# Kernel optimization log

Measured on AMD Instinct MI355X. Metric: run time of the kernel, lower is better.

The kernel has to match this reference:

```python
import jax, jax.numpy as jnp
import numpy as np


def setup_inputs() -> dict:
    key = jax.random.key(0)
    k1, k2 = jax.random.split(key)
    B, C, H, W_, P = 32, 256, 64, 64, 8
    x = jax.random.normal(k1, (B, C, H, W_), dtype=jnp.float32)
    # 1x1 conv weight [P, C] and bias [P], init like torch Conv2d default
    bound = 1.0 / np.sqrt(C)
    W = jax.random.uniform(k2, (P, C), dtype=jnp.float32, minval=-bound, maxval=bound)
    b = jnp.zeros((P,), dtype=jnp.float32)
    return {"x": x, "W": W, "b": b}


def reference(x, W, b):
    B, C, H, Wd = x.shape
    P = W.shape[0]
    # 1x1 conv: scores[b,p,h,w] = sum_c W[p,c] * x[b,c,h,w] + b[p]
    scores = jnp.einsum('pc,bchw->bphw', W, x) + b[None, :, None, None]
    # spatial softmax over HW
    part_maps = jax.nn.softmax(scores.reshape(B, P, H * Wd), axis=2).reshape(B, P, H, Wd)
    # fused per-part weighted average pool: mean over HW of x * map
    pooled = jnp.einsum('bchw,bphw->bpc', x, part_maps) / (H * Wd)  # [B,P,C]
    return pooled.reshape(B, P * C)
```

## Files before the change

kernel.cpp:

```cpp
#include <hip/hip_runtime.h>

#define HW 4096
#define NC 256
#define NP 8
#define NB 32
#define CHW 32
#define CPB 4
#define SPAN 128
#define NSPAN 32
#define NBLK (NB * NSPAN)

#define FMA4(acc, v, s)                  \
  acc.x = fmaf((v).x, (s), acc.x);       \
  acc.y = fmaf((v).y, (s), acc.y);       \
  acc.z = fmaf((v).z, (s), acc.z);       \
  acc.w = fmaf((v).w, (s), acc.w)

__global__ __launch_bounds__(256) void k_fused(
    const float* __restrict__ x, const float* __restrict__ Wm,
    const float* __restrict__ bias, float* __restrict__ partial,
    float* __restrict__ psum) {
  __shared__ __align__(16) float xs[NC][CHW];
  __shared__ __align__(16) float wt[NC][NP];
  __shared__ __align__(16) float sp[4][NP][CHW];
  __shared__ __align__(16) float els[NP][CHW];

  const int bid = blockIdx.x;
  const int b = bid >> 5;
  const int span = bid & 31;
  const int t = threadIdx.x, lane = t & 63, w = t >> 6;
  const float* xb = x + (size_t)b * NC * HW + span * SPAN;

#pragma unroll
  for (int p = 0; p < NP; ++p) wt[t][p] = Wm[p * NC + t];

  const int cr = lane >> 3;
  const int q = lane & 7;
  const int c0 = w << 6;
  const int ep = t >> 5, eh = t & 31;
  const int tk = t & 7;
  const float* xwp = xb + (size_t)(c0 + cr) * HW + q * 4;
  const float bia = bias[ep];

  float pacc[NP];
#pragma unroll
  for (int p = 0; p < NP; ++p) pacc[p] = 0.f;
  float esum_tot = 0.f;

  __syncthreads();

#pragma unroll 1
  for (int k = 0; k < CPB; ++k) {
    if (k) __syncthreads();

    float4 xv[8];
#pragma unroll
    for (int i = 0; i < 8; ++i)
      xv[i] = *(const float4*)(xwp + k * CHW + (size_t)(i * 8) * HW);

    float4 s4[NP];
#pragma unroll
    for (int p = 0; p < NP; ++p) s4[p] = make_float4(0.f, 0.f, 0.f, 0.f);
#pragma unroll
    for (int i = 0; i < 8; ++i) {
      const int c = c0 + i * 8 + cr;
      *(float4*)&xs[c][(q ^ cr) * 4] = xv[i];
      const float4 wA = *(const float4*)&wt[c][0];
      const float4 wB = *(const float4*)&wt[c][4];
      FMA4(s4[0], xv[i], wA.x);
      FMA4(s4[1], xv[i], wA.y);
      FMA4(s4[2], xv[i], wA.z);
      FMA4(s4[3], xv[i], wA.w);
      FMA4(s4[4], xv[i], wB.x);
      FMA4(s4[5], xv[i], wB.y);
      FMA4(s4[6], xv[i], wB.z);
      FMA4(s4[7], xv[i], wB.w);
    }

#pragma unroll
    for (int p = 0; p < NP; ++p) {
      float4 v = s4[p];
      v.x += __shfl_xor(v.x, 8);  v.y += __shfl_xor(v.y, 8);
      v.z += __shfl_xor(v.z, 8);  v.w += __shfl_xor(v.w, 8);
      v.x += __shfl_xor(v.x, 16); v.y += __shfl_xor(v.y, 16);
      v.z += __shfl_xor(v.z, 16); v.w += __shfl_xor(v.w, 16);
      v.x += __shfl_xor(v.x, 32); v.y += __shfl_xor(v.y, 32);
      v.z += __shfl_xor(v.z, 32); v.w += __shfl_xor(v.w, 32);
      if (cr == 0) *(float4*)&sp[w][p][q * 4] = v;
    }
    __syncthreads();

    {
      float a = bia;
#pragma unroll
      for (int ww = 0; ww < 4; ++ww) a += sp[ww][ep][eh];
      float e0 = expf(a);
      els[ep][eh] = e0;
      esum_tot += e0;
    }
    __syncthreads();

#pragma unroll
    for (int j = 0; j < 8; ++j) {
      const float4 xvb = *(const float4*)&xs[t][(j ^ tk) * 4];
#pragma unroll
      for (int p = 0; p < NP; ++p) {
        const float4 e4 = *(const float4*)&els[p][j * 4];
        pacc[p] = fmaf(xvb.x, e4.x, pacc[p]);
        pacc[p] = fmaf(xvb.y, e4.y, pacc[p]);
        pacc[p] = fmaf(xvb.z, e4.z, pacc[p]);
        pacc[p] = fmaf(xvb.w, e4.w, pacc[p]);
      }
    }
  }

#pragma unroll
  for (int p = 0; p < NP; ++p)
    partial[((size_t)bid * NP + p) * NC + t] = pacc[p];

#pragma unroll
  for (int off = 16; off; off >>= 1) esum_tot += __shfl_xor(esum_tot, off);
  if (eh == 0) psum[bid * NP + ep] = esum_tot;
}

__global__ __launch_bounds__(256) void k_reduce(
    const float* __restrict__ partial, const float* __restrict__ psum,
    float* __restrict__ out) {
  int bp = blockIdx.x;
  int b = bp >> 3, p = bp & 7;
  int t = threadIdx.x, lane = t & 63, w2 = t >> 6;

  __shared__ float gv;
  if (w2 == 0) {
    float v = (lane < NSPAN) ? psum[(size_t)(b * NSPAN + lane) * NP + p] : 0.f;
#pragma unroll
    for (int off = 16; off; off >>= 1) v += __shfl_xor(v, off);
    if (lane == 0) gv = 1.0f / (v * (float)HW);
  }
  __syncthreads();
  float ginv = gv;

  float acc = 0.f;
#pragma unroll
  for (int i = 0; i < NSPAN; ++i)
    acc += partial[(((size_t)b * NSPAN + i) * NP + p) * NC + t];
  out[((size_t)b * NP + p) * NC + t] = acc * ginv;
}

extern "C" void kernel_launch(void* const* d_in, const int* in_sizes, int n_in,
                              void* d_out, int out_size, void* d_ws, size_t ws_size,
                              hipStream_t stream) {
  const float* x = (const float*)d_in[0];
  const float* Wm = (const float*)d_in[1];
  const float* bias = (const float*)d_in[2];
  float* out = (float*)d_out;

  float* ws = (float*)d_ws;
  float* partial = ws;
  float* psum = ws + (size_t)NBLK * NP * NC;

  k_fused<<<NBLK, 256, 0, stream>>>(x, Wm, bias, partial, psum);
  k_reduce<<<NB * NP, 256, 0, stream>>>(partial, psum, out);
}
```

Baseline: 56.45 us.

## Pipeline x loads via async global_load_lds with 4-stage LDS ring, 512-thread blocks

Replaces register-staged x loads with direct global-to-LDS async loads, keeping three chunks in flight across a four-buffer ring with manual vmcnt waits and raw barriers. Blocks become 512 threads, each covering 512 spatial positions in 16 chunks, so the grid drops from 1024 to 256 blocks and the partial buffer and reduce work shrink. The intent is to hide HBM latency behind compute. The cost is more LDS per block, fewer blocks for occupancy, and fragile hand-written waitcnt logic.

```diff
diff --git a/kernel.cpp b/kernel.cpp
--- a/kernel.cpp
+++ b/kernel.cpp
@@ -1,14 +1,14 @@
 #include <hip/hip_runtime.h>
+#include <stdint.h>
 
 #define HW 4096
 #define NC 256
 #define NP 8
 #define NB 32
 #define CHW 32
-#define CPB 4
-#define SPAN 128
-#define NSPAN 32
-#define NBLK (NB * NSPAN)
+#define NCHK 16
+#define NOCT 8
+#define NBLK (NB * NOCT)
 
 #define FMA4(acc, v, s)                  \
   acc.x = fmaf((v).x, (s), acc.x);       \
@@ -16,111 +16,145 @@
   acc.z = fmaf((v).z, (s), acc.z);       \
   acc.w = fmaf((v).w, (s), acc.w)
 
-__global__ __launch_bounds__(256) void k_fused(
+__device__ __forceinline__ void gload_lds16(const float* g, float* l) {
+  __builtin_amdgcn_global_load_lds(
+      (const __attribute__((address_space(1))) uint32_t*)g,
+      (__attribute__((address_space(3))) uint32_t*)l, 16, 0, 0);
+}
+
+__global__ __launch_bounds__(512) void k_fused(
     const float* __restrict__ x, const float* __restrict__ Wm,
     const float* __restrict__ bias, float* __restrict__ partial,
     float* __restrict__ psum) {
-  __shared__ __align__(16) float xs[NC][CHW];
+  __shared__ __align__(16) float xs[4][NC][CHW];
   __shared__ __align__(16) float wt[NC][NP];
-  __shared__ __align__(16) float sp[4][NP][CHW];
+  __shared__ __align__(16) float sp[8][NP][CHW];
   __shared__ __align__(16) float els[NP][CHW];
 
   const int bid = blockIdx.x;
-  const int b = bid >> 5;
-  const int span = bid & 31;
+  const int b = bid >> 3;
+  const int oct = bid & 7;
   const int t = threadIdx.x, lane = t & 63, w = t >> 6;
-  const float* xb = x + (size_t)b * NC * HW + span * SPAN;
+  const float* xb = x + (size_t)b * NC * HW + oct * (NCHK * CHW);
 
 #pragma unroll
-  for (int p = 0; p < NP; ++p) wt[t][p] = Wm[p * NC + t];
+  for (int i = 0; i < 4; ++i) {
+    int idx = i * 512 + t;
+    wt[idx & 255][idx >> 8] = Wm[idx];
+  }
 
   const int cr = lane >> 3;
   const int q = lane & 7;
-  const int c0 = w << 6;
-  const int ep = t >> 5, eh = t & 31;
-  const int tk = t & 7;
-  const float* xwp = xb + (size_t)(c0 + cr) * HW + q * 4;
+  const int rbase = (w << 5) + cr;
+  const int sseg = (q ^ cr) << 2;
+  const float* gbase = xb + (size_t)rbase * HW + sseg;
+
+  const int ep = (t & 255) >> 5, eh = t & 31;
   const float bia = bias[ep];
+  const int brow = t >> 1, bh = (t & 1) * 4;
+  const int bx7 = brow & 7;
 
   float pacc[NP];
 #pragma unroll
   for (int p = 0; p < NP; ++p) pacc[p] = 0.f;
   float esum_tot = 0.f;
 
-  __syncthreads();
+#pragma unroll
+  for (int k0 = 0; k0 < 3; ++k0) {
+#pragma unroll
+    for (int i = 0; i < 4; ++i)
+      gload_lds16(gbase + (size_t)(i * 8) * HW + k0 * CHW,
+                  &xs[k0][(w << 5) + (i << 3)][0]);
+  }
 
 #pragma unroll 1
-  for (int k = 0; k < CPB; ++k) {
-    if (k) __syncthreads();
+  for (int k = 0; k < NCHK; ++k) {
+    if (k <= 13)      asm volatile("s_waitcnt vmcnt(8) lgkmcnt(0)" ::: "memory");
+    else if (k == 14) asm volatile("s_waitcnt vmcnt(4) lgkmcnt(0)" ::: "memory");
+    else              asm volatile("s_waitcnt vmcnt(0) lgkmcnt(0)" ::: "memory");
+    __builtin_amdgcn_s_barrier();
+    __builtin_amdgcn_sched_barrier(0);
 
-    float4 xv[8];
+    if (k + 3 < NCHK) {
+      const float* g = gbase + (size_t)((k + 3) * CHW);
 #pragma unroll
-    for (int i = 0; i < 8; ++i)
-      xv[i] = *(const float4*)(xwp + k * CHW + (size_t)(i * 8) * HW);
-
-    float4 s4[NP];
-#pragma unroll
-    for (int p = 0; p < NP; ++p) s4[p] = make_float4(0.f, 0.f, 0.f, 0.f);
-#pragma unroll
-    for (int i = 0; i < 8; ++i) {
-      const int c = c0 + i * 8 + cr;
-      *(float4*)&xs[c][(q ^ cr) * 4] = xv[i];
-      const float4 wA = *(const float4*)&wt[c][0];
-      const float4 wB = *(const float4*)&wt[c][4];
-      FMA4(s4[0], xv[i], wA.x);
-      FMA4(s4[1], xv[i], wA.y);
-      FMA4(s4[2], xv[i], wA.z);
-      FMA4(s4[3], xv[i], wA.w);
-      FMA4(s4[4], xv[i], wB.x);
-      FMA4(s4[5], xv[i], wB.y);
-      FMA4(s4[6], xv[i], wB.z);
-      FMA4(s4[7], xv[i], wB.w);
+      for (int i = 0; i < 4; ++i)
+        gload_lds16(g + (size_t)(i * 8) * HW,
+                    &xs[(k + 3) & 3][(w << 5) + (i << 3)][0]);
     }
 
-#pragma unroll
-    for (int p = 0; p < NP; ++p) {
-      float4 v = s4[p];
-      v.x += __shfl_xor(v.x, 8);  v.y += __shfl_xor(v.y, 8);
-      v.z += __shfl_xor(v.z, 8);  v.w += __shfl_xor(v.w, 8);
-      v.x += __shfl_xor(v.x, 16); v.y += __shfl_xor(v.y, 16);
-      v.z += __shfl_xor(v.z, 16); v.w += __shfl_xor(v.w, 16);
-      v.x += __shfl_xor(v.x, 32); v.y += __shfl_xor(v.y, 32);
-      v.z += __shfl_xor(v.z, 32); v.w += __shfl_xor(v.w, 32);
-      if (cr == 0) *(float4*)&sp[w][p][q * 4] = v;
-    }
-    __syncthreads();
+    const int buf = k & 3;
 
     {
+      float4 s4[NP];
+#pragma unroll
+      for (int p = 0; p < NP; ++p) s4[p] = make_float4(0.f, 0.f, 0.f, 0.f);
+#pragma unroll
+      for (int i = 0; i < 4; ++i) {
+        const int c = (w << 5) + (i << 3) + cr;
+        const float4 xv = *(const float4*)&xs[buf][c][sseg];
+        const float4 wA = *(const float4*)&wt[c][0];
+        const float4 wB = *(const float4*)&wt[c][4];
+        FMA4(s4[0], xv, wA.x);
+        FMA4(s4[1], xv, wA.y);
+        FMA4(s4[2], xv, wA.z);
+        FMA4(s4[3], xv, wA.w);
+        FMA4(s4[4], xv, wB.x);
+        FMA4(s4[5], xv, wB.y);
+        FMA4(s4[6], xv, wB.z);
+        FMA4(s4[7], xv, wB.w);
+      }
+#pragma unroll
+      for (int p = 0; p < NP; ++p) {
+        float4 v = s4[p];
+        v.x += __shfl_xor(v.x, 8);  v.y += __shfl_xor(v.y, 8);
+        v.z += __shfl_xor(v.z, 8);  v.w += __shfl_xor(v.w, 8);
+        v.x += __shfl_xor(v.x, 16); v.y += __shfl_xor(v.y, 16);
+        v.z += __shfl_xor(v.z, 16); v.w += __shfl_xor(v.w, 16);
+        v.x += __shfl_xor(v.x, 32); v.y += __shfl_xor(v.y, 32);
+        v.z += __shfl_xor(v.z, 32); v.w += __shfl_xor(v.w, 32);
+        if (cr == 0) *(float4*)&sp[w][p][q * 4] = v;
+      }
+    }
+    asm volatile("s_waitcnt lgkmcnt(0)" ::: "memory");
+    __builtin_amdgcn_s_barrier();
+
+    if (t < 256) {
       float a = bia;
 #pragma unroll
-      for (int ww = 0; ww < 4; ++ww) a += sp[ww][ep][eh];
-      float e0 = expf(a);
+      for (int ww = 0; ww < 8; ++ww) a += sp[ww][ep][eh];
+      const float e0 = expf(a);
       els[ep][eh] = e0;
       esum_tot += e0;
     }
-    __syncthreads();
+    asm volatile("s_waitcnt lgkmcnt(0)" ::: "memory");
+    __builtin_amdgcn_s_barrier();
 
 #pragma unroll
-    for (int j = 0; j < 8; ++j) {
-      const float4 xvb = *(const float4*)&xs[t][(j ^ tk) * 4];
+    for (int j = 0; j < 4; ++j) {
+      const int seg = bh + j;
+      const float4 xv = *(const float4*)&xs[buf][brow][(seg ^ bx7) << 2];
 #pragma unroll
       for (int p = 0; p < NP; ++p) {
-        const float4 e4 = *(const float4*)&els[p][j * 4];
-        pacc[p] = fmaf(xvb.x, e4.x, pacc[p]);
-        pacc[p] = fmaf(xvb.y, e4.y, pacc[p]);
-        pacc[p] = fmaf(xvb.z, e4.z, pacc[p]);
-        pacc[p] = fmaf(xvb.w, e4.w, pacc[p]);
+        const float4 e4 = *(const float4*)&els[p][seg << 2];
+        pacc[p] = fmaf(xv.x, e4.x, pacc[p]);
+        pacc[p] = fmaf(xv.y, e4.y, pacc[p]);
+        pacc[p] = fmaf(xv.z, e4.z, pacc[p]);
+        pacc[p] = fmaf(xv.w, e4.w, pacc[p]);
       }
     }
   }
 
 #pragma unroll
-  for (int p = 0; p < NP; ++p)
-    partial[((size_t)bid * NP + p) * NC + t] = pacc[p];
+  for (int p = 0; p < NP; ++p) {
+    float v = pacc[p] + __shfl_xor(pacc[p], 1);
+    if ((t & 1) == 0)
+      partial[((size_t)bid * NP + p) * NC + brow] = v;
+  }
 
 #pragma unroll
   for (int off = 16; off; off >>= 1) esum_tot += __shfl_xor(esum_tot, off);
-  if (eh == 0) psum[bid * NP + ep] = esum_tot;
+  if (t < 256 && eh == 0) psum[bid * NP + ep] = esum_tot;
 }
 
 __global__ __launch_bounds__(256) void k_reduce(
@@ -132,9 +166,9 @@
 
   __shared__ float gv;
   if (w2 == 0) {
-    float v = (lane < NSPAN) ? psum[(size_t)(b * NSPAN + lane) * NP + p] : 0.f;
+    float v = (lane < NOCT) ? psum[(size_t)(b * NOCT + lane) * NP + p] : 0.f;
 #pragma unroll
-    for (int off = 16; off; off >>= 1) v += __shfl_xor(v, off);
+    for (int off = 4; off; off >>= 1) v += __shfl_xor(v, off);
     if (lane == 0) gv = 1.0f / (v * (float)HW);
   }
   __syncthreads();
@@ -142,8 +176,8 @@
 
   float acc = 0.f;
 #pragma unroll
-  for (int i = 0; i < NSPAN; ++i)
-    acc += partial[(((size_t)b * NSPAN + i) * NP + p) * NC + t];
+  for (int i = 0; i < NOCT; ++i)
+    acc += partial[(((size_t)b * NOCT + i) * NP + p) * NC + t];
   out[((size_t)b * NP + p) * NC + t] = acc * ginv;
 }
 
@@ -159,6 +193,6 @@
   float* partial = ws;
   float* psum = ws + (size_t)NBLK * NP * NC;
 
-  k_fused<<<NBLK, 256, 0, stream>>>(x, Wm, bias, partial, psum);
+  k_fused<<<NBLK, 512, 0, stream>>>(x, Wm, bias, partial, psum);
   k_reduce<<<NB * NP, 256, 0, stream>>>(partial, psum, out);
 }
```

New measurement: 82.88 us. +46.8%, slower.

## Double-buffer x tiles with async global-to-LDS loads and halve block count

Applied to the files above, without the earlier changes.

Replaces the register-staged loads of x with `__builtin_amdgcn_global_load_lds` direct-to-LDS transfers into a double-buffered shared tile. The next 32-column chunk is prefetched while the current one is processed, so global memory latency overlaps the score, exp and pooling math. Each block now covers a 256-pixel span instead of 128, which halves the block count and the partial sums the reduce kernel must read. The costs are double the LDS for x, an extra barrier per chunk, fewer blocks available to hide latency, and reliance on the compiler to insert the right waits before the barriers that guard the async writes.

```diff
diff --git a/kernel.cpp b/kernel.cpp
--- a/kernel.cpp
+++ b/kernel.cpp
@@ -1,13 +1,14 @@
 #include <hip/hip_runtime.h>
+#include <stdint.h>
 
 #define HW 4096
 #define NC 256
 #define NP 8
 #define NB 32
 #define CHW 32
-#define CPB 4
-#define SPAN 128
-#define NSPAN 32
+#define NCHK 8
+#define SPAN 256
+#define NSPAN 16
 #define NBLK (NB * NSPAN)
 
 #define FMA4(acc, v, s)                  \
@@ -16,30 +17,38 @@
   acc.z = fmaf((v).z, (s), acc.z);       \
   acc.w = fmaf((v).w, (s), acc.w)
 
+__device__ __forceinline__ void gload_lds16(const float* g, float* l) {
+  __builtin_amdgcn_global_load_lds(
+      (const __attribute__((address_space(1))) uint32_t*)g,
+      (__attribute__((address_space(3))) uint32_t*)l, 16, 0, 0);
+}
+
 __global__ __launch_bounds__(256) void k_fused(
     const float* __restrict__ x, const float* __restrict__ Wm,
     const float* __restrict__ bias, float* __restrict__ partial,
     float* __restrict__ psum) {
-  __shared__ __align__(16) float xs[NC][CHW];
+  __shared__ __align__(16) float xs[2][NC][CHW];
   __shared__ __align__(16) float wt[NC][NP];
   __shared__ __align__(16) float sp[4][NP][CHW];
   __shared__ __align__(16) float els[NP][CHW];
 
   const int bid = blockIdx.x;
-  const int b = bid >> 5;
-  const int span = bid & 31;
+  const int b = bid >> 4;
+  const int span = bid & 15;
   const int t = threadIdx.x, lane = t & 63, w = t >> 6;
   const float* xb = x + (size_t)b * NC * HW + span * SPAN;
 
 #pragma unroll
   for (int p = 0; p < NP; ++p) wt[t][p] = Wm[p * NC + t];
 
+  const int srow = lane >> 3;
+  const int sseg = (lane & 7) ^ srow;
+  const float* gst = xb + (size_t)((w << 6) + srow) * HW + sseg * 4;
+
   const int cr = lane >> 3;
   const int q = lane & 7;
-  const int c0 = w << 6;
   const int ep = t >> 5, eh = t & 31;
   const int tk = t & 7;
-  const float* xwp = xb + (size_t)(c0 + cr) * HW + q * 4;
   const float bia = bias[ep];
 
   float pacc[NP];
@@ -47,46 +56,52 @@
   for (int p = 0; p < NP; ++p) pacc[p] = 0.f;
   float esum_tot = 0.f;
 
+#pragma unroll
+  for (int ii = 0; ii < 8; ++ii)
+    gload_lds16(gst + (size_t)(ii << 3) * HW, &xs[0][(w << 6) + (ii << 3)][0]);
   __syncthreads();
 
 #pragma unroll 1
-  for (int k = 0; k < CPB; ++k) {
-    if (k) __syncthreads();
+  for (int k = 0; k < NCHK; ++k) {
+    const int cb = k & 1;
 
-    float4 xv[8];
+    if (k + 1 < NCHK) {
+      const float* g = gst + (size_t)(k + 1) * CHW;
 #pragma unroll
-    for (int i = 0; i < 8; ++i)
-      xv[i] = *(const float4*)(xwp + k * CHW + (size_t)(i * 8) * HW);
-
-    float4 s4[NP];
-#pragma unroll
-    for (int p = 0; p < NP; ++p) s4[p] = make_float4(0.f, 0.f, 0.f, 0.f);
-#pragma unroll
-    for (int i = 0; i < 8; ++i) {
-      const int c = c0 + i * 8 + cr;
-      *(float4*)&xs[c][(q ^ cr) * 4] = xv[i];
-      const float4 wA = *(const float4*)&wt[c][0];
-      const float4 wB = *(const float4*)&wt[c][4];
-      FMA4(s4[0], xv[i], wA.x);
-      FMA4(s4[1], xv[i], wA.y);
-      FMA4(s4[2], xv[i], wA.z);
-      FMA4(s4[3], xv[i], wA.w);
-      FMA4(s4[4], xv[i], wB.x);
-      FMA4(s4[5], xv[i], wB.y);
-      FMA4(s4[6], xv[i], wB.z);
-      FMA4(s4[7], xv[i], wB.w);
+      for (int ii = 0; ii < 8; ++ii)
+        gload_lds16(g + (size_t)(ii << 3) * HW, &xs[cb ^ 1][(w << 6) + (ii << 3)][0]);
     }
 
+    {
+      float4 s4[NP];
 #pragma unroll
-    for (int p = 0; p < NP; ++p) {
-      float4 v = s4[p];
-      v.x += __shfl_xor(v.x, 8);  v.y += __shfl_xor(v.y, 8);
-      v.z += __shfl_xor(v.z, 8);  v.w += __shfl_xor(v.w, 8);
-      v.x += __shfl_xor(v.x, 16); v.y += __shfl_xor(v.y, 16);
-      v.z += __shfl_xor(v.z, 16); v.w += __shfl_xor(v.w, 16);
-      v.x += __shfl_xor(v.x, 32); v.y += __shfl_xor(v.y, 32);
-      v.z += __shfl_xor(v.z, 32); v.w += __shfl_xor(v.w, 32);
-      if (cr == 0) *(float4*)&sp[w][p][q * 4] = v;
+      for (int p = 0; p < NP; ++p) s4[p] = make_float4(0.f, 0.f, 0.f, 0.f);
+#pragma unroll
+      for (int i = 0; i < 8; ++i) {
+        const int c = (w << 6) + (i << 3) + cr;
+        const float4 xv = *(const float4*)&xs[cb][c][(q ^ cr) << 2];
+        const float4 wA = *(const float4*)&wt[c][0];
+        const float4 wB = *(const float4*)&wt[c][4];
+        FMA4(s4[0], xv, wA.x);
+        FMA4(s4[1], xv, wA.y);
+        FMA4(s4[2], xv, wA.z);
+        FMA4(s4[3], xv, wA.w);
+        FMA4(s4[4], xv, wB.x);
+        FMA4(s4[5], xv, wB.y);
+        FMA4(s4[6], xv, wB.z);
+        FMA4(s4[7], xv, wB.w);
+      }
+#pragma unroll
+      for (int p = 0; p < NP; ++p) {
+        float4 v = s4[p];
+        v.x += __shfl_xor(v.x, 8);  v.y += __shfl_xor(v.y, 8);
+        v.z += __shfl_xor(v.z, 8);  v.w += __shfl_xor(v.w, 8);
+        v.x += __shfl_xor(v.x, 16); v.y += __shfl_xor(v.y, 16);
+        v.z += __shfl_xor(v.z, 16); v.w += __shfl_xor(v.w, 16);
+        v.x += __shfl_xor(v.x, 32); v.y += __shfl_xor(v.y, 32);
+        v.z += __shfl_xor(v.z, 32); v.w += __shfl_xor(v.w, 32);
+        if (cr == 0) *(float4*)&sp[w][p][q * 4] = v;
+      }
     }
     __syncthreads();
 
@@ -94,7 +109,7 @@
       float a = bia;
 #pragma unroll
       for (int ww = 0; ww < 4; ++ww) a += sp[ww][ep][eh];
-      float e0 = expf(a);
+      const float e0 = expf(a);
       els[ep][eh] = e0;
       esum_tot += e0;
     }
@@ -102,16 +117,17 @@
 
 #pragma unroll
     for (int j = 0; j < 8; ++j) {
-      const float4 xvb = *(const float4*)&xs[t][(j ^ tk) * 4];
+      const float4 xv = *(const float4*)&xs[cb][t][(j ^ tk) << 2];
 #pragma unroll
       for (int p = 0; p < NP; ++p) {
         const float4 e4 = *(const float4*)&els[p][j * 4];
-        pacc[p] = fmaf(xvb.x, e4.x, pacc[p]);
-        pacc[p] = fmaf(xvb.y, e4.y, pacc[p]);
-        pacc[p] = fmaf(xvb.z, e4.z, pacc[p]);
-        pacc[p] = fmaf(xvb.w, e4.w, pacc[p]);
+        pacc[p] = fmaf(xv.x, e4.x, pacc[p]);
+        pacc[p] = fmaf(xv.y, e4.y, pacc[p]);
+        pacc[p] = fmaf(xv.z, e4.z, pacc[p]);
+        pacc[p] = fmaf(xv.w, e4.w, pacc[p]);
       }
     }
+    __syncthreads();
   }
 
 #pragma unroll
@@ -134,7 +150,7 @@
   if (w2 == 0) {
     float v = (lane < NSPAN) ? psum[(size_t)(b * NSPAN + lane) * NP + p] : 0.f;
 #pragma unroll
-    for (int off = 16; off; off >>= 1) v += __shfl_xor(v, off);
+    for (int off = 8; off; off >>= 1) v += __shfl_xor(v, off);
     if (lane == 0) gv = 1.0f / (v * (float)HW);
   }
   __syncthreads();
```

Result: slower. 58.17 us (+3.0%).
